# Kernel optimization log

Measured on AMD Instinct MI355X. Metric: run time of the kernel, lower is better.

## Reference

```python
import jax, jax.numpy as jnp
import numpy as np

B, T, C = 4, 2048, 1024
H = 16
D = C // H  # head_dim = 64


def setup_inputs() -> dict:
    key = jax.random.key(0)
    ks = jax.random.split(key, 5)
    scale_in = 1.0 / np.sqrt(C)
    x = jax.random.normal(ks[0], (B, T, C), dtype=jnp.float32)
    w_qkv = jax.random.normal(ks[1], (C, 3 * C), dtype=jnp.float32) * scale_in
    b_qkv = jnp.zeros((3 * C,), dtype=jnp.float32)
    w_proj = jax.random.normal(ks[2], (C, C), dtype=jnp.float32) * scale_in
    b_proj = jnp.zeros((C,), dtype=jnp.float32)
    return {"x": x, "w_qkv": w_qkv, "b_qkv": b_qkv, "w_proj": w_proj, "b_proj": b_proj}


def reference(x, w_qkv, b_qkv, w_proj, b_proj):
    # fused QKV projection: [B,T,3C]
    qkv = x @ w_qkv + b_qkv
    q, k, v = jnp.split(qkv, 3, axis=-1)
    # [B,T,C] -> [B,H,T,D]
    q = q.reshape(B, T, H, D).transpose(0, 2, 1, 3)
    k = k.reshape(B, T, H, D).transpose(0, 2, 1, 3)
    v = v.reshape(B, T, H, D).transpose(0, 2, 1, 3)
    scale = 1.0 / np.sqrt(D)
    scores = jnp.einsum('bhqd,bhkd->bhqk', q, k) * scale  # [B,H,T,T]
    causal = jnp.tril(jnp.ones((T, T), dtype=bool))
    scores = jnp.where(causal, scores, jnp.finfo(scores.dtype).min)
    attn = jax.nn.softmax(scores, axis=-1)
    y = jnp.einsum('bhqk,bhkd->bhqd', attn, v)  # [B,H,T,D]
    y = y.transpose(0, 2, 1, 3).reshape(B, T, C)
    return y @ w_proj + b_proj
```

## Files before the change

### kernel.cpp

```cpp
#include <hip/hip_runtime.h>

typedef unsigned short u16;
typedef unsigned int u32;
typedef unsigned long long u64;
typedef __attribute__((ext_vector_type(8))) short s16x8;
typedef __attribute__((ext_vector_type(4))) float f32x4;

#if __has_builtin(__builtin_amdgcn_exp2f)
#define EXP2(x) __builtin_amdgcn_exp2f(x)
#else
#define EXP2(x) __expf((x) * 0.69314718f)
#endif

#if __has_builtin(__builtin_amdgcn_rcpf)
#define RCP(x) __builtin_amdgcn_rcpf(x)
#else
#define RCP(x) (1.0f / (x))
#endif

#define GLL(gp, lp) __builtin_amdgcn_global_load_lds(                         \
    (const __attribute__((address_space(1))) unsigned int*)(const void*)(gp), \
    (__attribute__((address_space(3))) unsigned int*)(void*)(lp), 16, 0, 0)

__device__ __forceinline__ u16 f2bf(float f) {
    union { float f; u32 u; } v; v.f = f;
    u32 r = v.u + 0x7FFF + ((v.u >> 16) & 1);
    return (u16)(r >> 16);
}

__device__ __forceinline__ u32 pack2_trunc(float a, float b) {
    union { float f; u32 u; } x, y; x.f = a; y.f = b;
    return (x.u >> 16) | (y.u & 0xFFFF0000u);
}

__device__ __forceinline__ float bf2f(u16 b) {
    union { u32 u; float f; } v; v.u = ((u32)b) << 16;
    return v.f;
}

__device__ __forceinline__ s16x8 scale_frag(s16x8 v, float s) {
    s16x8 o;
#pragma unroll
    for (int i = 0; i < 8; i++) o[i] = (short)f2bf(bf2f((u16)v[i]) * s);
    return o;
}

__global__ __launch_bounds__(256) void cast_f32_bf16(const float* __restrict__ in,
                                                     u16* __restrict__ out) {
    size_t i = ((size_t)blockIdx.x * 256 + threadIdx.x) * 4;
    float4 f = *(const float4*)(in + i);
    u16 o[4] = { f2bf(f.x), f2bf(f.y), f2bf(f.z), f2bf(f.w) };
    *(unsigned long long*)(out + i) =
        (unsigned long long)o[0] | ((unsigned long long)o[1] << 16) |
        ((unsigned long long)o[2] << 32) | ((unsigned long long)o[3] << 48);
}

__global__ __launch_bounds__(256) void transpose_cast(const float* __restrict__ in,
                                                      u16* __restrict__ out,
                                                      int rows, int cols) {
    __shared__ float tile[32][33];
    int c0 = blockIdx.x * 32, r0 = blockIdx.y * 32;
    int tx = threadIdx.x, ty = threadIdx.y;
    for (int i = 0; i < 32; i += 8)
        tile[ty + i][tx] = in[(size_t)(r0 + ty + i) * cols + (c0 + tx)];
    __syncthreads();
    for (int i = 0; i < 32; i += 8)
        out[(size_t)(c0 + ty + i) * rows + (r0 + tx)] = f2bf(tile[tx][ty + i]);
}

template<int MODE, int NB>
__global__ __launch_bounds__(256, 4) void gemm_bt64(const u16* __restrict__ A,
                                                    const u16* __restrict__ BT,
                                                    const float* __restrict__ bias,
                                                    void* __restrict__ O1,
                                                    u16* __restrict__ vT,
                                                    int M, int N, int K) {
    __shared__ u16 SMEM[18432];
    u16* As = SMEM;
    u16* Bs = SMEM + 8192;
    int id = blockIdx.x;
    int xcd = id & 7, s = id >> 3;
    int ni = s % NB, mi8 = s / NB;
    int n0 = ni * 128, m0 = (xcd * 8 + mi8) * 128;
    int tid = threadIdx.x, lane = tid & 63, w = tid >> 6;
    int row16 = lane & 15, quad = lane >> 4;
    int wm = (w >> 1) * 64, wn = (w & 1) * 64;
    f32x4 acc[4][4] = {};

    int lr = lane >> 3;
    int cswz = (lane & 7) ^ lr;
    const u16* Ag = A + (size_t)(m0 + w * 32 + lr) * K + cswz * 8;
    const u16* Bg = BT + (size_t)(n0 + w * 32 + lr) * K + cswz * 8;
    u16* Asl = As + (w * 32) * 64;
    u16* Bsl = Bs + (w * 32) * 64;

    for (int k0 = 0; k0 < K; k0 += 64) {
        __syncthreads();
#pragma unroll
        for (int j = 0; j < 4; j++) {
            GLL(Ag + k0 + (size_t)j * 8 * K, Asl + j * 8 * 64);
            GLL(Bg + k0 + (size_t)j * 8 * K, Bsl + j * 8 * 64);
        }
        __syncthreads();
#pragma unroll
        for (int kk = 0; kk < 2; kk++) {
            s16x8 af[4], bf[4];
#pragma unroll
            for (int mi = 0; mi < 4; mi++)
                af[mi] = *(const s16x8*)&As[(wm + mi * 16 + row16) * 64 +
                                            (((kk * 4 + quad) ^ (row16 & 7)) * 8)];
#pragma unroll
            for (int ni2 = 0; ni2 < 4; ni2++)
                bf[ni2] = *(const s16x8*)&Bs[(wn + ni2 * 16 + row16) * 64 +
                                             (((kk * 4 + quad) ^ (row16 & 7)) * 8)];
#pragma unroll
            for (int mi = 0; mi < 4; mi++)
#pragma unroll
                for (int ni2 = 0; ni2 < 4; ni2++)
                    acc[mi][ni2] = __builtin_amdgcn_mfma_f32_16x16x32_bf16(
                        af[mi], bf[ni2], acc[mi][ni2], 0, 0, 0);
        }
    }

    if (MODE == 0) {
        float* O = (float*)O1;
#pragma unroll
        for (int ni2 = 0; ni2 < 4; ni2++) {
            int col = n0 + wn + ni2 * 16 + row16;
            float bv = bias[col];
#pragma unroll
            for (int mi = 0; mi < 4; mi++)
#pragma unroll
                for (int r = 0; r < 4; r++)
                    O[(size_t)(m0 + wm + mi * 16 + quad * 4 + r) * N + col] =
                        acc[mi][ni2][r] + bv;
        }
    } else if (n0 < 2048) {
        u16* qk = (u16*)O1;
#pragma unroll
        for (int ni2 = 0; ni2 < 4; ni2++) {
            int col = n0 + wn + ni2 * 16 + row16;
            float bv = bias[col];
#pragma unroll
            for (int mi = 0; mi < 4; mi++)
#pragma unroll
                for (int r = 0; r < 4; r++)
                    qk[(size_t)(m0 + wm + mi * 16 + quad * 4 + r) * 2048 + col] =
                        f2bf(acc[mi][ni2][r] + bv);
        }
    } else {
        __syncthreads();
        u16* scr = SMEM + w * 64 * 72;
#pragma unroll
        for (int ni2 = 0; ni2 < 4; ni2++) {
            float bv = bias[n0 + wn + ni2 * 16 + row16];
#pragma unroll
            for (int mi = 0; mi < 4; mi++)
#pragma unroll
                for (int r = 0; r < 4; r++)
                    scr[(ni2 * 16 + row16) * 72 + (mi * 16 + quad * 4 + r)] =
                        f2bf(acc[mi][ni2][r] + bv);
        }
        __syncthreads();
        int r8 = lane >> 3, c8 = lane & 7;
        int vbase = (m0 >> 11) * 1024 + (n0 - 2048) + wn;
        int tb = (m0 & 2047) + wm;
#pragma unroll
        for (int it = 0; it < 8; it++) {
            s16x8 vv = *(const s16x8*)&scr[(it * 8 + r8) * 72 + c8 * 8];
            *(s16x8*)&vT[(size_t)(vbase + it * 8 + r8) * 2048 + tb + c8 * 8] = vv;
        }
    }
}

__global__ __launch_bounds__(256, 2) void attn_kernel(const u16* __restrict__ qk,
                                                      const u16* __restrict__ vT,
                                                      u16* __restrict__ y) {
    __shared__ u16 Kb[2][4096];
    __shared__ u16 Vb[2][4096];
    __shared__ u16 Ps[4][2048];

    int tid = threadIdx.x, lane = tid & 63, w = tid >> 6;
    int row16 = lane & 15, quad = lane >> 4;
    int id = blockIdx.x;
    int xcd = id & 7, slot = id >> 3;
    int qt = 15 - (slot >> 3);
    int bh = ((slot & 7) << 3) | xcd;
    int b = bh >> 4, h = bh & 15;
    const u16* qkb = qk + (size_t)b * 2048 * 2048;
    const u16* vtb = vT + ((size_t)(b * 1024) + h * 64) * 2048;

    int lr = lane >> 3, cswz = (lane & 7) ^ lr;
    const u16* Kg = qkb + (size_t)(w * 16 + lr) * 2048 + 1024 + h * 64 + cswz * 8;
    const u16* Vg = vtb + (size_t)(w * 16 + lr) * 2048 + cswz * 8;
    u16* Psw = Ps[w];
    int sw = row16 & 7;

    s16x8 ones;
#pragma unroll
    for (int i = 0; i < 8; i++) ones[i] = (short)0x3F80;
    const float qs = 0.125f * 1.44269504f;

    int q0 = qt * 128;
    int niter = 2 * qt + 2;
    int qw = q0 + w * 32;

    s16x8 qf[2][2];
#pragma unroll
    for (int mi = 0; mi < 2; mi++) {
        const u16* qp = qkb + (size_t)(qw + mi * 16 + row16) * 2048 + h * 64 + quad * 8;
        qf[mi][0] = scale_frag(*(const s16x8*)qp, qs);
        qf[mi][1] = scale_frag(*(const s16x8*)(qp + 32), qs);
    }

    f32x4 acc_o[2][4] = {};
    f32x4 acc_l[2] = {};

#pragma unroll
    for (int j = 0; j < 2; j++) {
        GLL(Kg + (size_t)j * 8 * 2048, Kb[0] + w * 16 * 64 + j * 8 * 64);
        GLL(Vg + (size_t)j * 8 * 2048, Vb[0] + w * 16 * 64 + j * 8 * 64);
    }

    for (int kb = 0; kb < niter; kb++) {
        int cur = kb & 1;
        __syncthreads();
        if (kb + 1 < niter) {
            int k1 = (kb + 1) * 64;
#pragma unroll
            for (int j = 0; j < 2; j++) {
                GLL(Kg + (size_t)(k1 + j * 8) * 2048, Kb[cur ^ 1] + w * 16 * 64 + j * 8 * 64);
                GLL(Vg + k1 + (size_t)j * 8 * 2048, Vb[cur ^ 1] + w * 16 * 64 + j * 8 * 64);
            }
        }
        int k0 = kb * 64;
        if (k0 > qw + 31) continue;
        const u16* Kc = Kb[cur];
        const u16* Vc = Vb[cur];

        f32x4 sc[2][4];
#pragma unroll
        for (int nk = 0; nk < 4; nk++) {
            s16x8 kf0 = *(const s16x8*)&Kc[(nk * 16 + row16) * 64 + ((quad ^ sw) * 8)];
            s16x8 kf1 = *(const s16x8*)&Kc[(nk * 16 + row16) * 64 + (((4 + quad) ^ sw) * 8)];
#pragma unroll
            for (int mi = 0; mi < 2; mi++) {
                f32x4 z = {};
                z = __builtin_amdgcn_mfma_f32_16x16x32_bf16(kf0, qf[mi][0], z, 0, 0, 0);
                z = __builtin_amdgcn_mfma_f32_16x16x32_bf16(kf1, qf[mi][1], z, 0, 0, 0);
                sc[mi][nk] = z;
            }
        }
        if (k0 + 63 > qw) {
#pragma unroll
            for (int mi = 0; mi < 2; mi++) {
                int qg = qw + mi * 16 + row16;
#pragma unroll
                for (int nk = 0; nk < 4; nk++) {
                    int kbase = k0 + nk * 16 + quad * 4;
#pragma unroll
                    for (int r = 0; r < 4; r++)
                        if (kbase + r > qg) sc[mi][nk][r] = -__builtin_inff();
                }
            }
        }
#pragma unroll
        for (int mi = 0; mi < 2; mi++)
#pragma unroll
            for (int nk = 0; nk < 4; nk++) {
                float p0 = EXP2(sc[mi][nk][0]);
                float p1 = EXP2(sc[mi][nk][1]);
                float p2 = EXP2(sc[mi][nk][2]);
                float p3 = EXP2(sc[mi][nk][3]);
                u32 w0 = pack2_trunc(p0, p1);
                u32 w1 = pack2_trunc(p2, p3);
                int u = nk * 2 + (quad >> 1);
                int eo = ((u ^ sw) * 8) + (quad & 1) * 4;
                *(u64*)&Psw[mi * 1024 + row16 * 64 + eo] = (u64)w0 | ((u64)w1 << 32);
            }
#pragma unroll
        for (int kk = 0; kk < 2; kk++) {
            int co = ((kk * 4 + quad) ^ sw) * 8;
            s16x8 pf0 = *(const s16x8*)&Psw[row16 * 64 + co];
            s16x8 pf1 = *(const s16x8*)&Psw[1024 + row16 * 64 + co];
#pragma unroll
            for (int nd = 0; nd < 4; nd++) {
                s16x8 vf = *(const s16x8*)&Vc[(nd * 16 + row16) * 64 + co];
                acc_o[0][nd] = __builtin_amdgcn_mfma_f32_16x16x32_bf16(pf0, vf, acc_o[0][nd], 0, 0, 0);
                acc_o[1][nd] = __builtin_amdgcn_mfma_f32_16x16x32_bf16(pf1, vf, acc_o[1][nd], 0, 0, 0);
            }
            acc_l[0] = __builtin_amdgcn_mfma_f32_16x16x32_bf16(pf0, ones, acc_l[0], 0, 0, 0);
            acc_l[1] = __builtin_amdgcn_mfma_f32_16x16x32_bf16(pf1, ones, acc_l[1], 0, 0, 0);
        }
    }

#pragma unroll
    for (int mi = 0; mi < 2; mi++) {
        int t0 = qw + mi * 16 + quad * 4;
#pragma unroll
        for (int r = 0; r < 4; r++) {
            float inv = RCP(acc_l[mi][r]);
#pragma unroll
            for (int nd = 0; nd < 4; nd++)
                y[((size_t)b * 2048 + t0 + r) * 1024 + h * 64 + nd * 16 + row16] =
                    f2bf(acc_o[mi][nd][r] * inv);
        }
    }
}

extern "C" void kernel_launch(void* const* d_in, const int* in_sizes, int n_in,
                              void* d_out, int out_size, void* d_ws, size_t ws_size,
                              hipStream_t stream) {
    const float* x      = (const float*)d_in[0];
    const float* w_qkv  = (const float*)d_in[1];
    const float* b_qkv  = (const float*)d_in[2];
    const float* w_proj = (const float*)d_in[3];
    const float* b_proj = (const float*)d_in[4];
    float* out = (float*)d_out;

    u16* ws     = (u16*)d_ws;
    u16* x_bf   = ws;
    u16* wqkvT  = x_bf  + (size_t)8192 * 1024;
    u16* wprojT = wqkvT + (size_t)3072 * 1024;
    u16* qkbuf  = wprojT + (size_t)1024 * 1024;
    u16* vT     = qkbuf + (size_t)8192 * 2048;
    u16* ybf    = vT    + (size_t)4096 * 2048;

    cast_f32_bf16<<<dim3(8192), dim3(256), 0, stream>>>(x, x_bf);
    transpose_cast<<<dim3(96, 32), dim3(32, 8), 0, stream>>>(w_qkv, wqkvT, 1024, 3072);
    transpose_cast<<<dim3(32, 32), dim3(32, 8), 0, stream>>>(w_proj, wprojT, 1024, 1024);
    gemm_bt64<1, 24><<<dim3(1536), 256, 0, stream>>>(x_bf, wqkvT, b_qkv, (void*)qkbuf, vT, 8192, 3072, 1024);
    attn_kernel<<<dim3(1024), 256, 0, stream>>>(qkbuf, vT, ybf);
    gemm_bt64<0, 8><<<dim3(512), 256, 0, stream>>>(ybf, wprojT, b_proj, (void*)out, nullptr, 8192, 1024, 1024);
}
```

Before: 234.4 us.

## Replace QKV GEMM with 256x256-tile, 8-wave pipelined kernel

Adds a dedicated QKV projection kernel that uses 256x256 output tiles with 512 threads, double-buffered LDS, and staggered global-to-LDS loads interleaved with MFMA phases, using barriers and setprio to keep the matrix units busy. Larger tiles raise arithmetic intensity and cut global traffic compared with the 128x128 generic GEMM. The V epilogue transposes through LDS scratch before writing vT. It uses 128KB of LDS and more registers per block, which lowers occupancy, and the hand-written wait counts are fragile.

```diff
diff --git a/kernel.cpp b/kernel.cpp
--- a/kernel.cpp
+++ b/kernel.cpp
@@ -66,6 +66,163 @@
     __syncthreads();
     for (int i = 0; i < 32; i += 8)
         out[(size_t)(c0 + ty + i) * rows + (r0 + tx)] = f2bf(tile[tx][ty + i]);
+}
+
+__global__ __launch_bounds__(512, 2) void gemm_qkv_8p(const u16* __restrict__ A,
+                                                      const u16* __restrict__ BT,
+                                                      const float* __restrict__ bias,
+                                                      u16* __restrict__ qk,
+                                                      u16* __restrict__ vT) {
+    constexpr int K = 1024;
+    __shared__ u16 SM[65536];
+    u16* As = SM;
+    u16* Bs = SM + 32768;
+
+    int id = blockIdx.x;
+    int xcd = id & 7, j = id >> 3;
+    int m0 = (xcd * 4 + j / 12) * 256;
+    int n0 = (j % 12) * 256;
+
+    int tid = threadIdx.x, lane = tid & 63, w = tid >> 6;
+    int row16 = lane & 15, quad = lane >> 4;
+    int wm = w >> 2, wn = w & 3;
+    int lr = lane >> 3, c8 = lane & 7;
+    int cswz = c8 ^ lr;
+
+    const u16* srcA[4];
+    const u16* srcB[4];
+#pragma unroll
+    for (int q = 0; q < 4; q++)
+        srcA[q] = A + (size_t)(m0 + q * 64 + w * 8 + lr) * K + cswz * 8;
+#pragma unroll
+    for (int u = 0; u < 4; u++) {
+        int pr = u * 64 + w * 8 + lr;
+        int c = ((pr >> 5) & 3) * 64 + (pr >> 7) * 32 + (pr & 31);
+        srcB[u] = BT + (size_t)(n0 + c) * K + cswz * 8;
+    }
+    int ldsW = w * 512;
+
+    int aBase = (wm * 128 + row16) * 64;
+    int bBase = (wn * 32 + row16) * 64;
+    int cx0 = (quad ^ (row16 & 7)) * 8;
+    int cx1 = ((4 + quad) ^ (row16 & 7)) * 8;
+
+    f32x4 acc[8][4] = {};
+
+#define STGA(Q, KO, BUFD) GLL(srcA[Q] + (KO), As + (BUFD) * 16384 + (Q) * 4096 + ldsW)
+#define STGB(U, KO, BUFD) GLL(srcB[U] + (KO), Bs + (BUFD) * 16384 + (U) * 4096 + ldsW)
+#define BAR __builtin_amdgcn_s_barrier();
+#define WAITL                                                                  \
+    asm volatile("s_waitcnt lgkmcnt(0)" ::: "memory");                         \
+    __builtin_amdgcn_sched_barrier(0);
+#define VM6 asm volatile("s_waitcnt vmcnt(6)" ::: "memory")
+#define VM0 asm volatile("s_waitcnt vmcnt(0)" ::: "memory")
+#define VMN (void)0
+#define LOADA(BUF, MH)                                                         \
+    _Pragma("unroll") for (int m4 = 0; m4 < 4; m4++) {                         \
+        afr[m4][0] = *(const s16x8*)&As[(BUF) * 16384 + aBase + ((MH) * 64 + m4 * 16) * 64 + cx0]; \
+        afr[m4][1] = *(const s16x8*)&As[(BUF) * 16384 + aBase + ((MH) * 64 + m4 * 16) * 64 + cx1]; \
+    }
+#define LOADB(BUF, NH)                                                         \
+    _Pragma("unroll") for (int nn = 0; nn < 2; nn++) {                         \
+        bfr[(NH) * 2 + nn][0] = *(const s16x8*)&Bs[(BUF) * 16384 + bBase + ((NH) * 128 + nn * 16) * 64 + cx0]; \
+        bfr[(NH) * 2 + nn][1] = *(const s16x8*)&Bs[(BUF) * 16384 + bBase + ((NH) * 128 + nn * 16) * 64 + cx1]; \
+    }
+#define MFMA8(NH, MH)                                                          \
+    __builtin_amdgcn_s_setprio(1);                                             \
+    _Pragma("unroll") for (int m4 = 0; m4 < 4; m4++)                           \
+        _Pragma("unroll") for (int nn = 0; nn < 2; nn++) {                     \
+            f32x4& ac = acc[(MH) * 4 + m4][(NH) * 2 + nn];                     \
+            ac = __builtin_amdgcn_mfma_f32_16x16x32_bf16(afr[m4][0], bfr[(NH) * 2 + nn][0], ac, 0, 0, 0); \
+            ac = __builtin_amdgcn_mfma_f32_16x16x32_bf16(afr[m4][1], bfr[(NH) * 2 + nn][1], ac, 0, 0, 0); \
+        }                                                                      \
+    __builtin_amdgcn_s_setprio(0);
+
+#define TILE(KT, BUF, S1, S2, EW)                                              \
+  {                                                                            \
+    const int k1 = ((KT) + 1) * 64, k2 = ((KT) + 2) * 64;                      \
+    s16x8 afr[4][2], bfr[4][2];                                                \
+    LOADA(BUF, 0)                                                              \
+    LOADB(BUF, 0)                                                              \
+    if (S1) { STGA(1, k1, (BUF) ^ 1); STGA(3, k1, (BUF) ^ 1); }                \
+    BAR WAITL MFMA8(0, 0) BAR                                                  \
+    LOADB(BUF, 1)                                                              \
+    if (S2) { STGB(0, k2, BUF); STGB(1, k2, BUF); }                            \
+    BAR WAITL MFMA8(1, 0) BAR                                                  \
+    LOADA(BUF, 1)                                                              \
+    if (S2) { STGB(2, k2, BUF); STGB(3, k2, BUF); }                            \
+    BAR WAITL MFMA8(0, 1) BAR                                                  \
+    if (S2) { STGA(0, k2, BUF); STGA(2, k2, BUF); }                            \
+    BAR WAITL MFMA8(1, 1)                                                      \
+    __builtin_amdgcn_sched_barrier(0);                                         \
+    EW;                                                                        \
+    BAR                                                                        \
+  }
+
+#pragma unroll
+    for (int q = 0; q < 4; q++) STGA(q, 0, 0);
+#pragma unroll
+    for (int u = 0; u < 4; u++) STGB(u, 0, 0);
+#pragma unroll
+    for (int u = 0; u < 4; u++) STGB(u, 64, 1);
+    STGA(0, 64, 1);
+    STGA(2, 64, 1);
+    VM6;
+    BAR
+
+    for (int kt = 0; kt < 14; kt += 2) {
+        TILE(kt, 0, 1, 1, VM6)
+        TILE(kt + 1, 1, 1, 1, VM6)
+    }
+    TILE(14, 0, 1, 0, VM0)
+    TILE(15, 1, 0, 0, VMN)
+
+    if (n0 < 2048) {
+#pragma unroll
+        for (int ni = 0; ni < 4; ni++) {
+            int col = n0 + wn * 64 + ni * 16 + row16;
+            float bv = bias[col];
+#pragma unroll
+            for (int mi = 0; mi < 8; mi++)
+#pragma unroll
+                for (int r = 0; r < 4; r++)
+                    qk[(size_t)(m0 + wm * 128 + mi * 16 + quad * 4 + r) * 2048 + col] =
+                        f2bf(acc[mi][ni][r] + bv);
+        }
+    } else {
+        int b = m0 >> 11;
+        int colV0 = (n0 - 2048) + wn * 64;
+        u16* scr = SM + w * 4608;
+        __syncthreads();
+#pragma unroll
+        for (int mh = 0; mh < 2; mh++) {
+#pragma unroll
+            for (int ni = 0; ni < 4; ni++) {
+                float bv = bias[n0 + wn * 64 + ni * 16 + row16];
+#pragma unroll
+                for (int m4 = 0; m4 < 4; m4++)
+#pragma unroll
+                    for (int r = 0; r < 4; r++)
+                        scr[(ni * 16 + row16) * 72 + (m4 * 16 + quad * 4 + r)] =
+                            f2bf(acc[mh * 4 + m4][ni][r] + bv);
+            }
+            __syncthreads();
+            int tb = (m0 & 2047) + wm * 128 + mh * 64;
+#pragma unroll
+            for (int it = 0; it < 8; it++) {
+                s16x8 vv = *(const s16x8*)&scr[(it * 8 + lr) * 72 + c8 * 8];
+                *(s16x8*)&vT[(size_t)(b * 1024 + colV0 + it * 8 + lr) * 2048 + tb + c8 * 8] = vv;
+            }
+            if (mh == 0) __syncthreads();
+        }
+    }
+#undef TILE
+#undef MFMA8
+#undef LOADA
+#undef LOADB
+#undef STGA
+#undef STGB
+#undef WAITL
 }
 
 template<int MODE, int NB>
@@ -329,7 +486,7 @@
     cast_f32_bf16<<<dim3(8192), dim3(256), 0, stream>>>(x, x_bf);
     transpose_cast<<<dim3(96, 32), dim3(32, 8), 0, stream>>>(w_qkv, wqkvT, 1024, 3072);
     transpose_cast<<<dim3(32, 32), dim3(32, 8), 0, stream>>>(w_proj, wprojT, 1024, 1024);
-    gemm_bt64<1, 24><<<dim3(1536), 256, 0, stream>>>(x_bf, wqkvT, b_qkv, (void*)qkbuf, vT, 8192, 3072, 1024);
+    gemm_qkv_8p<<<dim3(384), dim3(512), 0, stream>>>(x_bf, wqkvT, b_qkv, qkbuf, vT);
     attn_kernel<<<dim3(1024), 256, 0, stream>>>(qkbuf, vT, ybf);
     gemm_bt64<0, 8><<<dim3(512), 256, 0, stream>>>(ybf, wprojT, b_proj, (void*)out, nullptr, 8192, 1024, 1024);
 }
```

New measurement: 231.6 us. Within noise of the previous version (-1.2%).
